# Kernel optimization log

Hardware: AMD Instinct MI355X
Metric: run time of the kernel (lower is better)

Reference implementation:

```python
import jax, jax.numpy as jnp
import numpy as np

N_SAMPLES = 2 ** 15  # 32768
NYQUIST = 22050.0 / 2.0
MIN_FREQ = 40.0 / NYQUIST
MAX_FREQ = 4000.0 / NYQUIST
FREQ_RANGE = MAX_FREQ - MIN_FREQ


def interp_linear(x, out_size):
    """torch F.interpolate(mode='linear', align_corners=False) along last axis."""
    in_size = x.shape[-1]
    scale = in_size / out_size
    coords = (jnp.arange(out_size, dtype=x.dtype) + 0.5) * scale - 0.5
    coords = jnp.clip(coords, 0.0, in_size - 1)
    lo = jnp.floor(coords).astype(jnp.int32)
    hi = jnp.minimum(lo + 1, in_size - 1)
    w = coords - lo.astype(x.dtype)
    return x[..., lo] * (1.0 - w) + x[..., hi] * w


def translate(pair, shift, scale):
    # angle of complex(pair[:,:,0], pair[:,:,1]) / pi, then affine
    angle = jnp.arctan2(pair[:, :, 1, :], pair[:, :, 0, :]) / np.pi
    return shift + angle * scale


def setup_inputs() -> dict:
    key = jax.random.key(0)
    k1, k2 = jax.random.split(key)
    x = jax.random.normal(k1, (16, 8, 10, 128), dtype=jnp.float32)
    noise = jax.random.normal(k2, (16, 8, N_SAMPLES), dtype=jnp.float32)
    return {"x": x, "noise": noise}


def reference(x, noise):
    # x: (batch, n_osc, 10, time_ctrl); noise: (batch, n_osc, N_SAMPLES)
    basic = x[:, :, 0:2, :]
    amp = jnp.sqrt(jnp.sum(basic * basic, axis=2))            # (b, o, t)
    amp = interp_linear(amp, N_SAMPLES)                       # (b, o, N)

    f0 = translate(basic, MIN_FREQ, FREQ_RANGE)               # control-rate
    mix = interp_linear(translate(x[:, :, 2:4, :], 1.0, 0.5), N_SAMPLES)
    harm_amp = amp * mix
    noise_amp = amp * (1.0 - mix)

    noise_std = translate(x[:, :, 4:6, :], MIN_FREQ, FREQ_RANGE)
    mod_factor = translate(x[:, :, 6:8, :], 0.25, 4.75)
    b = translate(x[:, :, 8:10, :], 0.1, 9.9)

    # band_filtered_noise: narrowband noise as a frequency-jittered sine
    f0_fr = interp_linear(f0, N_SAMPLES)
    std_fr = interp_linear(noise_std, N_SAMPLES)
    bfn = jnp.sin(jnp.cumsum(f0_fr + noise * std_fr, axis=-1))
    noise_sig = noise_amp * bfn

    mod_factor = interp_linear(mod_factor, N_SAMPLES)
    b = interp_linear(b, N_SAMPLES)
    mod = b * jnp.sin(jnp.cumsum(mod_factor, axis=-1))
    sig = harm_amp * jnp.sin(jnp.cumsum(f0_fr, axis=-1) + mod)

    mixed = noise_sig + sig                                   # (b, o, N)
    return jnp.mean(mixed, axis=1, keepdims=True)             # (b, 1, N)
```

## Files before the change

### kernel.cpp

```cpp
#include <hip/hip_runtime.h>
#include <math.h>

#define NS    32768
#define NB    128
#define NSEQ  128
#define TPB1  256
#define NPART 32
#define PART  (NS / NPART)
#define TPB2  256
#define CH    4

__device__ __forceinline__ float fsin(double x) {
    double u = x * 0.15915494309189533576888376337251;
    double f = u - rint(u);
    return __builtin_amdgcn_sinf((float)f);
}

__device__ __forceinline__ void seg_params(int ci0, int& lo, int& hi,
                                           double& w0, double& wst) {
    if (ci0 < 128)            { lo = 0;   hi = 1;   w0 = 0.0; wst = 0.0; }
    else if (ci0 >= NS - 128) { lo = 127; hi = 127; w0 = 0.0; wst = 0.0; }
    else {
        lo = (ci0 - 128) >> 8;  hi = lo + 1;
        int off = (ci0 - 128) & 255;
        w0 = (off + 0.5) * (1.0 / 256.0);
        wst = 1.0 / 256.0;
    }
}

__global__ __launch_bounds__(TPB1)
void pre_kernel(const float* __restrict__ xg, const float* __restrict__ ng,
                double* __restrict__ wacc, double* __restrict__ wbins) {
    __shared__ double bins[6][NB];
    __shared__ double lred[TPB1 / 64][3];

    const double PI_  = 3.14159265358979323846;
    const double MINF = 40.0 / 11025.0;
    const double FRNG = (4000.0 - 40.0) / 11025.0;

    int s    = blockIdx.x;
    int tid  = threadIdx.x;
    int lane = tid & 63;
    int wid  = tid >> 6;

    const float* xs = xg + s * 10 * 128;
    double* gb = wbins + (size_t)s * 6 * NB;
    for (int idx = tid; idx < 6 * NB; idx += TPB1) {
        int q = idx >> 7, j = idx & 127;
        double v;
        if (q == 0) {
            double a0 = (double)xs[j], a1 = (double)xs[128 + j];
            v = sqrt(a0 * a0 + a1 * a1);
        } else {
            int c = (q - 1) * 2;
            double yy = (double)xs[(c + 1) * 128 + j];
            double xx = (double)xs[c * 128 + j];
            double ang = atan2(yy, xx) / PI_;
            double sh, sc;
            if      (q == 1) { sh = MINF; sc = FRNG; }
            else if (q == 2) { sh = 1.0;  sc = 0.5;  }
            else if (q == 3) { sh = MINF; sc = FRNG; }
            else if (q == 4) { sh = 0.25; sc = 4.75; }
            else             { sh = 0.1;  sc = 9.9;  }
            v = sh + ang * sc;
        }
        bins[q][j] = v;
        gb[q * NB + j] = v;
    }
    __syncthreads();

    int c   = tid;
    int ci0 = c * 128;
    int lo, hi; double w0, wst;
    seg_params(ci0, lo, hi, w0, wst);
    double f0L = bins[1][lo], dF0 = bins[1][hi] - f0L;
    double stL = bins[3][lo], dSt = bins[3][hi] - stL;
    double mfL = bins[4][lo], dMf = bins[4][hi] - mfL;

    const float4* nn4 = reinterpret_cast<const float4*>(ng + (size_t)s * NS + ci0);
    double S0 = 0.0, S1 = 0.0;
    #pragma unroll
    for (int q4 = 0; q4 < 32; ++q4) {
        float4 nv = nn4[q4];
        double jd = (double)(q4 * 4);
        S0 += (double)nv.x; S1 += jd * (double)nv.x;
        S0 += (double)nv.y; S1 += (jd + 1.0) * (double)nv.y;
        S0 += (double)nv.z; S1 += (jd + 2.0) * (double)nv.z;
        S0 += (double)nv.w; S1 += (jd + 3.0) * (double)nv.w;
    }
    double sw = 128.0 * w0 + wst * 8128.0;
    double t3 = 128.0 * f0L + dF0 * sw;
    double t2 = 128.0 * mfL + dMf * sw;
    double t1 = t3 + stL * S0 + dSt * (w0 * S0 + wst * S1);

    double v1 = t1, v3 = t3, v2 = t2;
    #pragma unroll
    for (int d = 1; d < 64; d <<= 1) {
        double u1 = __shfl_up(v1, d);
        double u3 = __shfl_up(v3, d);
        double u2 = __shfl_up(v2, d);
        if (lane >= d) { v1 += u1; v3 += u3; v2 += u2; }
    }
    if (lane == 63) { lred[wid][0] = v1; lred[wid][1] = v3; lred[wid][2] = v2; }
    __syncthreads();
    double b1 = 0.0, b3 = 0.0, b2 = 0.0;
    #pragma unroll
    for (int k = 0; k < TPB1 / 64 - 1; ++k)
        if (wid > k) { b1 += lred[k][0]; b3 += lred[k][1]; b2 += lred[k][2]; }

    if ((c & 7) == 0) {
        double* A = wacc + ((size_t)s * NPART + (c >> 3)) * 3;
        A[0] = b1 + (v1 - t1);
        A[1] = b3 + (v3 - t3);
        A[2] = b2 + (v2 - t2);
    }
}

__global__ __launch_bounds__(TPB2)
void fm_main_kernel(const float* __restrict__ ng, const double* __restrict__ wacc,
                    const double* __restrict__ wbins, float* __restrict__ out) {
    __shared__ double lbins[8][6][NB];
    __shared__ double lred[TPB2 / 64][3];

    int bx   = blockIdx.x;
    int b    = bx >> 5;
    int p    = bx & (NPART - 1);
    int tid  = threadIdx.x;
    int lane = tid & 63;
    int wid  = tid >> 6;

    const double* gb = wbins + (size_t)b * 8 * 6 * NB;
    double* lb = &lbins[0][0][0];
    for (int idx = tid; idx < 8 * 6 * NB; idx += TPB2) lb[idx] = gb[idx];
    __syncthreads();

    int i0 = p * PART + tid * CH;
    int lo, hi; double w0, wst;
    seg_params(i0, lo, hi, w0, wst);

    float acc[CH] = {0.f, 0.f, 0.f, 0.f};

    for (int h = 0; h < 8; ++h) {
        int s = b * 8 + h;
        const double* B = &lbins[h][0][0];
        double amL = B[0 * NB + lo], dAm = B[0 * NB + hi] - amL;
        double f0L = B[1 * NB + lo], dF0 = B[1 * NB + hi] - f0L;
        double mxL = B[2 * NB + lo], dMx = B[2 * NB + hi] - mxL;
        double stL = B[3 * NB + lo], dSt = B[3 * NB + hi] - stL;
        double mfL = B[4 * NB + lo], dMf = B[4 * NB + hi] - mfL;
        double bL  = B[5 * NB + lo], dB  = B[5 * NB + hi] - bL;

        float4 nv = *reinterpret_cast<const float4*>(ng + (size_t)s * NS + i0);
        double n0 = (double)nv.x, n1 = (double)nv.y, n2 = (double)nv.z, n3 = (double)nv.w;
        double S0 = n0 + n1 + n2 + n3;
        double S1 = n1 + 2.0 * n2 + 3.0 * n3;

        double sw = 4.0 * w0 + wst * 6.0;
        double T3 = 4.0 * f0L + dF0 * sw;
        double T2 = 4.0 * mfL + dMf * sw;
        double T1 = T3 + stL * S0 + dSt * (w0 * S0 + wst * S1);

        double v1 = T1, v3 = T3, v2 = T2;
        #pragma unroll
        for (int d = 1; d < 64; d <<= 1) {
            double u1 = __shfl_up(v1, d);
            double u3 = __shfl_up(v3, d);
            double u2 = __shfl_up(v2, d);
            if (lane >= d) { v1 += u1; v3 += u3; v2 += u2; }
        }
        if (lane == 63) { lred[wid][0] = v1; lred[wid][1] = v3; lred[wid][2] = v2; }
        __syncthreads();
        double b1 = 0.0, b3 = 0.0, b2 = 0.0;
        #pragma unroll
        for (int k = 0; k < TPB2 / 64 - 1; ++k)
            if (wid > k) { b1 += lred[k][0]; b3 += lred[k][1]; b2 += lred[k][2]; }
        __syncthreads();

        const double* A = wacc + ((size_t)s * NPART + p) * 3;
        double a1 = A[0] + b1 + (v1 - T1);
        double a3 = A[1] + b3 + (v3 - T3);
        double a2 = A[2] + b2 + (v2 - T2);

        float nf[CH] = {nv.x, nv.y, nv.z, nv.w};
        double w = w0;
        #pragma unroll
        for (int j = 0; j < CH; ++j) {
            double nd  = (double)nf[j];
            double f0v = f0L + w * dF0;
            double stv = stL + w * dSt;
            double mfv = mfL + w * dMf;
            a1 += f0v + nd * stv;
            a3 += f0v;
            a2 += mfv;
            double ampv = amL + w * dAm;
            double mixv = mxL + w * dMx;
            double bv   = bL  + w * dB;
            double harm = ampv * mixv;
            double namp = ampv * (1.0 - mixv);
            float s1 = fsin(a1);
            float s2 = fsin(a2);
            float s3 = fsin(a3 + bv * (double)s2);
            acc[j] += (float)namp * s1 + (float)harm * s3;
            w += wst;
        }
    }

    float4 o = make_float4(acc[0] * 0.125f, acc[1] * 0.125f,
                           acc[2] * 0.125f, acc[3] * 0.125f);
    *reinterpret_cast<float4*>(out + (size_t)b * NS + i0) = o;
}

extern "C" void kernel_launch(void* const* d_in, const int* in_sizes, int n_in,
                              void* d_out, int out_size, void* d_ws, size_t ws_size,
                              hipStream_t stream) {
    const float* x     = (const float*)d_in[0];
    const float* noise = (const float*)d_in[1];
    float* out = (float*)d_out;
    double* wacc  = (double*)d_ws;
    double* wbins = wacc + (size_t)NSEQ * NPART * 3;
    pre_kernel<<<NSEQ, TPB1, 0, stream>>>(x, noise, wacc, wbins);
    fm_main_kernel<<<16 * NPART, TPB2, 0, stream>>>(noise, wacc, wbins, out);
}
```

Baseline: 95.86 us.

## Precompute per-16-sample phase offsets and run main synthesis in fp32

The pre-kernel now computes exclusive prefix phase sums at 16-sample granularity using 1024 threads, with phases pre-scaled by 1/(2π) and reduced modulo 1. This removes the per-oscillator block-wide double scans and barriers from the main kernel. The main kernel instead assigns one thread per (cell, oscillator), does the local accumulation and interpolation in fp32, and sums the 8 oscillators with xor shuffles. It trades double-precision work and syncs for more workspace traffic and fp32 rounding inside each cell.

```diff
diff --git a/kernel.cpp b/kernel.cpp
--- a/kernel.cpp
+++ b/kernel.cpp
@@ -4,25 +4,24 @@
 #define NS    32768
 #define NB    128
 #define NSEQ  128
-#define TPB1  256
-#define NPART 32
-#define PART  (NS / NPART)
+#define CELL  16
+#define NCELL (NS / CELL)
+#define TPB1  1024
+#define RUN   (NS / TPB1)
 #define TPB2  256
-#define CH    4
-
-__device__ __forceinline__ float fsin(double x) {
-    double u = x * 0.15915494309189533576888376337251;
-    double f = u - rint(u);
-    return __builtin_amdgcn_sinf((float)f);
-}
-
-__device__ __forceinline__ void seg_params(int ci0, int& lo, int& hi,
+#define GRID2 (16 * NCELL * 8 / TPB2)
+
+__device__ __forceinline__ float sinr(float x) {
+    return __builtin_amdgcn_sinf(x - rintf(x));
+}
+
+__device__ __forceinline__ void seg_params(int i, int& lo, int& hi,
                                            double& w0, double& wst) {
-    if (ci0 < 128)            { lo = 0;   hi = 1;   w0 = 0.0; wst = 0.0; }
-    else if (ci0 >= NS - 128) { lo = 127; hi = 127; w0 = 0.0; wst = 0.0; }
+    if (i < 128)            { lo = 0;   hi = 1;   w0 = 0.0; wst = 0.0; }
+    else if (i >= NS - 128) { lo = 127; hi = 127; w0 = 0.0; wst = 0.0; }
     else {
-        lo = (ci0 - 128) >> 8;  hi = lo + 1;
-        int off = (ci0 - 128) & 255;
+        lo = (i - 128) >> 8;  hi = lo + 1;
+        int off = (i - 128) & 255;
         w0 = (off + 0.5) * (1.0 / 256.0);
         wst = 1.0 / 256.0;
     }
@@ -30,32 +29,31 @@
 
 __global__ __launch_bounds__(TPB1)
 void pre_kernel(const float* __restrict__ xg, const float* __restrict__ ng,
-                double* __restrict__ wacc, double* __restrict__ wbins) {
-    __shared__ double bins[6][NB];
+                double* __restrict__ wacc, float* __restrict__ wbins) {
+    __shared__ double bf0[NB], bst[NB], bmf[NB];
     __shared__ double lred[TPB1 / 64][3];
 
-    const double PI_  = 3.14159265358979323846;
-    const double MINF = 40.0 / 11025.0;
-    const double FRNG = (4000.0 - 40.0) / 11025.0;
+    const double PI_    = 3.14159265358979323846;
+    const double INV2PI = 0.15915494309189533576888376337251;
+    const double MINF   = 40.0 / 11025.0;
+    const double FRNG   = (4000.0 - 40.0) / 11025.0;
 
     int s    = blockIdx.x;
     int tid  = threadIdx.x;
     int lane = tid & 63;
     int wid  = tid >> 6;
 
-    const float* xs = xg + s * 10 * 128;
-    double* gb = wbins + (size_t)s * 6 * NB;
-    for (int idx = tid; idx < 6 * NB; idx += TPB1) {
-        int q = idx >> 7, j = idx & 127;
+    const float* xs = xg + s * 10 * NB;
+    if (tid < 6 * NB) {
+        int q = tid >> 7, j = tid & 127;
         double v;
         if (q == 0) {
-            double a0 = (double)xs[j], a1 = (double)xs[128 + j];
+            double a0 = (double)xs[j], a1 = (double)xs[NB + j];
             v = sqrt(a0 * a0 + a1 * a1);
         } else {
-            int c = (q - 1) * 2;
-            double yy = (double)xs[(c + 1) * 128 + j];
-            double xx = (double)xs[c * 128 + j];
-            double ang = atan2(yy, xx) / PI_;
+            int c2 = (q - 1) * 2;
+            double ang = atan2((double)xs[(c2 + 1) * NB + j],
+                               (double)xs[c2 * NB + j]) / PI_;
             double sh, sc;
             if      (q == 1) { sh = MINF; sc = FRNG; }
             else if (q == 2) { sh = 1.0;  sc = 0.5;  }
@@ -63,37 +61,46 @@
             else if (q == 4) { sh = 0.25; sc = 4.75; }
             else             { sh = 0.1;  sc = 9.9;  }
             v = sh + ang * sc;
+            if (q != 2) v *= INV2PI;
         }
-        bins[q][j] = v;
-        gb[q * NB + j] = v;
+        wbins[s * (6 * NB) + tid] = (float)v;
+        if      (q == 1) bf0[j] = v;
+        else if (q == 3) bst[j] = v;
+        else if (q == 4) bmf[j] = v;
     }
     __syncthreads();
 
-    int c   = tid;
-    int ci0 = c * 128;
+    int ci = tid * RUN;
     int lo, hi; double w0, wst;
-    seg_params(ci0, lo, hi, w0, wst);
-    double f0L = bins[1][lo], dF0 = bins[1][hi] - f0L;
-    double stL = bins[3][lo], dSt = bins[3][hi] - stL;
-    double mfL = bins[4][lo], dMf = bins[4][hi] - mfL;
-
-    const float4* nn4 = reinterpret_cast<const float4*>(ng + (size_t)s * NS + ci0);
-    double S0 = 0.0, S1 = 0.0;
-    #pragma unroll
-    for (int q4 = 0; q4 < 32; ++q4) {
-        float4 nv = nn4[q4];
-        double jd = (double)(q4 * 4);
-        S0 += (double)nv.x; S1 += jd * (double)nv.x;
-        S0 += (double)nv.y; S1 += (jd + 1.0) * (double)nv.y;
-        S0 += (double)nv.z; S1 += (jd + 2.0) * (double)nv.z;
-        S0 += (double)nv.w; S1 += (jd + 3.0) * (double)nv.w;
-    }
-    double sw = 128.0 * w0 + wst * 8128.0;
-    double t3 = 128.0 * f0L + dF0 * sw;
-    double t2 = 128.0 * mfL + dMf * sw;
-    double t1 = t3 + stL * S0 + dSt * (w0 * S0 + wst * S1);
-
-    double v1 = t1, v3 = t3, v2 = t2;
+    seg_params(ci, lo, hi, w0, wst);
+    double f0L = bf0[lo], dF0 = bf0[hi] - f0L;
+    double stL = bst[lo], dSt = bst[hi] - stL;
+    double mfL = bmf[lo], dMf = bmf[hi] - mfL;
+
+    const float4* nn4 = reinterpret_cast<const float4*>(ng + (size_t)s * NS + ci);
+    double t1c[2], t3c[2], t2c[2];
+    #pragma unroll
+    for (int c = 0; c < 2; ++c) {
+        double S0 = 0.0, S1 = 0.0;
+        #pragma unroll
+        for (int q4 = 0; q4 < 4; ++q4) {
+            float4 nv = nn4[c * 4 + q4];
+            double jd = (double)(q4 * 4);
+            S0 += (double)nv.x; S1 += jd * (double)nv.x;
+            S0 += (double)nv.y; S1 += (jd + 1.0) * (double)nv.y;
+            S0 += (double)nv.z; S1 += (jd + 2.0) * (double)nv.z;
+            S0 += (double)nv.w; S1 += (jd + 3.0) * (double)nv.w;
+        }
+        double wc = w0 + (double)(c * 16) * wst;
+        double sw = 16.0 * wc + wst * 120.0;
+        double t3 = 16.0 * f0L + dF0 * sw;
+        double t2 = 16.0 * mfL + dMf * sw;
+        double t1 = t3 + stL * S0 + dSt * (wc * S0 + wst * S1);
+        t1c[c] = t1; t3c[c] = t3; t2c[c] = t2;
+    }
+    double r1 = t1c[0] + t1c[1], r3 = t3c[0] + t3c[1], r2 = t2c[0] + t2c[1];
+
+    double v1 = r1, v3 = r3, v2 = r2;
     #pragma unroll
     for (int d = 1; d < 64; d <<= 1) {
         double u1 = __shfl_up(v1, d);
@@ -104,110 +111,84 @@
     if (lane == 63) { lred[wid][0] = v1; lred[wid][1] = v3; lred[wid][2] = v2; }
     __syncthreads();
     double b1 = 0.0, b3 = 0.0, b2 = 0.0;
-    #pragma unroll
-    for (int k = 0; k < TPB1 / 64 - 1; ++k)
-        if (wid > k) { b1 += lred[k][0]; b3 += lred[k][1]; b2 += lred[k][2]; }
-
-    if ((c & 7) == 0) {
-        double* A = wacc + ((size_t)s * NPART + (c >> 3)) * 3;
-        A[0] = b1 + (v1 - t1);
-        A[1] = b3 + (v3 - t3);
-        A[2] = b2 + (v2 - t2);
-    }
+    for (int k = 0; k < wid; ++k) {
+        b1 += lred[k][0]; b3 += lred[k][1]; b2 += lred[k][2];
+    }
+    double e1 = b1 + v1 - r1, e3 = b3 + v3 - r3, e2 = b2 + v2 - r2;
+
+    double* A = wacc + ((size_t)s * NCELL + (size_t)tid * 2) * 3;
+    A[0] = e1;          A[1] = e3;          A[2] = e2;
+    A[3] = e1 + t1c[0]; A[4] = e3 + t3c[0]; A[5] = e2 + t2c[0];
 }
 
 __global__ __launch_bounds__(TPB2)
-void fm_main_kernel(const float* __restrict__ ng, const double* __restrict__ wacc,
-                    const double* __restrict__ wbins, float* __restrict__ out) {
-    __shared__ double lbins[8][6][NB];
-    __shared__ double lred[TPB2 / 64][3];
-
-    int bx   = blockIdx.x;
-    int b    = bx >> 5;
-    int p    = bx & (NPART - 1);
-    int tid  = threadIdx.x;
-    int lane = tid & 63;
-    int wid  = tid >> 6;
-
-    const double* gb = wbins + (size_t)b * 8 * 6 * NB;
-    double* lb = &lbins[0][0][0];
-    for (int idx = tid; idx < 8 * 6 * NB; idx += TPB2) lb[idx] = gb[idx];
-    __syncthreads();
-
-    int i0 = p * PART + tid * CH;
-    int lo, hi; double w0, wst;
-    seg_params(i0, lo, hi, w0, wst);
-
-    float acc[CH] = {0.f, 0.f, 0.f, 0.f};
-
-    for (int h = 0; h < 8; ++h) {
-        int s = b * 8 + h;
-        const double* B = &lbins[h][0][0];
-        double amL = B[0 * NB + lo], dAm = B[0 * NB + hi] - amL;
-        double f0L = B[1 * NB + lo], dF0 = B[1 * NB + hi] - f0L;
-        double mxL = B[2 * NB + lo], dMx = B[2 * NB + hi] - mxL;
-        double stL = B[3 * NB + lo], dSt = B[3 * NB + hi] - stL;
-        double mfL = B[4 * NB + lo], dMf = B[4 * NB + hi] - mfL;
-        double bL  = B[5 * NB + lo], dB  = B[5 * NB + hi] - bL;
-
-        float4 nv = *reinterpret_cast<const float4*>(ng + (size_t)s * NS + i0);
-        double n0 = (double)nv.x, n1 = (double)nv.y, n2 = (double)nv.z, n3 = (double)nv.w;
-        double S0 = n0 + n1 + n2 + n3;
-        double S1 = n1 + 2.0 * n2 + 3.0 * n3;
-
-        double sw = 4.0 * w0 + wst * 6.0;
-        double T3 = 4.0 * f0L + dF0 * sw;
-        double T2 = 4.0 * mfL + dMf * sw;
-        double T1 = T3 + stL * S0 + dSt * (w0 * S0 + wst * S1);
-
-        double v1 = T1, v3 = T3, v2 = T2;
+void fm2_kernel(const float* __restrict__ ng, const double* __restrict__ wacc,
+                const float* __restrict__ wbins, float* __restrict__ out) {
+    int g  = blockIdx.x * TPB2 + threadIdx.x;
+    int h  = g & 7;
+    int q  = g >> 3;
+    int b  = q >> 11;
+    int c  = q & (NCELL - 1);
+    int s  = (b << 3) + h;
+    int i0 = c << 4;
+
+    int lo, hi; double w0d, wstd;
+    seg_params(i0, lo, hi, w0d, wstd);
+    float w0  = (float)w0d;
+    float wsf = (float)wstd;
+
+    const float* B = wbins + s * (6 * NB);
+    float amL = B[lo],          dAm = B[hi] - amL;
+    float f0L = B[NB + lo],     dF0 = B[NB + hi] - f0L;
+    float mxL = B[2 * NB + lo], dMx = B[2 * NB + hi] - mxL;
+    float stL = B[3 * NB + lo], dSt = B[3 * NB + hi] - stL;
+    float mfL = B[4 * NB + lo], dMf = B[4 * NB + hi] - mfL;
+    float bbL = B[5 * NB + lo], dBb = B[5 * NB + hi] - bbL;
+
+    const double* A = wacc + ((size_t)s * NCELL + c) * 3;
+    double a1 = A[0], a3 = A[1], a2 = A[2];
+    float fr1 = (float)(a1 - rint(a1));
+    float fr3 = (float)(a3 - rint(a3));
+    float fr2 = (float)(a2 - rint(a2));
+
+    const float4* nn4 = reinterpret_cast<const float4*>(ng + (size_t)s * NS + i0);
+    float4 nv0 = nn4[0], nv1 = nn4[1], nv2 = nn4[2], nv3 = nn4[3];
+    float nf[CELL] = {nv0.x, nv0.y, nv0.z, nv0.w, nv1.x, nv1.y, nv1.z, nv1.w,
+                      nv2.x, nv2.y, nv2.z, nv2.w, nv3.x, nv3.y, nv3.z, nv3.w};
+
+    float arr[CELL];
+    float d1 = 0.f, d2 = 0.f, d3 = 0.f;
+    #pragma unroll
+    for (int j = 0; j < CELL; ++j) {
+        float wf  = fmaf((float)j, wsf, w0);
+        float f0v = fmaf(wf, dF0, f0L);
+        float stv = fmaf(wf, dSt, stL);
+        float mfv = fmaf(wf, dMf, mfL);
+        d3 += f0v;
+        d1 += fmaf(nf[j], stv, f0v);
+        d2 += mfv;
+        float ampv = fmaf(wf, dAm, amL);
+        float mixv = fmaf(wf, dMx, mxL);
+        float bv   = fmaf(wf, dBb, bbL);
+        float s2 = sinr(fr2 + d2);
+        float s1 = sinr(fr1 + d1);
+        float s3 = sinr(fmaf(bv, s2, fr3 + d3));
+        float harm = ampv * mixv;
+        arr[j] = fmaf(harm, s3, (ampv - harm) * s1);
+    }
+
+    #pragma unroll
+    for (int m = 1; m <= 4; m <<= 1) {
         #pragma unroll
-        for (int d = 1; d < 64; d <<= 1) {
-            double u1 = __shfl_up(v1, d);
-            double u3 = __shfl_up(v3, d);
-            double u2 = __shfl_up(v2, d);
-            if (lane >= d) { v1 += u1; v3 += u3; v2 += u2; }
-        }
-        if (lane == 63) { lred[wid][0] = v1; lred[wid][1] = v3; lred[wid][2] = v2; }
-        __syncthreads();
-        double b1 = 0.0, b3 = 0.0, b2 = 0.0;
+        for (int j = 0; j < CELL; ++j) arr[j] += __shfl_xor(arr[j], m);
+    }
+    if (h == 0) {
+        float4* op = reinterpret_cast<float4*>(out + (size_t)b * NS + i0);
         #pragma unroll
-        for (int k = 0; k < TPB2 / 64 - 1; ++k)
-            if (wid > k) { b1 += lred[k][0]; b3 += lred[k][1]; b2 += lred[k][2]; }
-        __syncthreads();
-
-        const double* A = wacc + ((size_t)s * NPART + p) * 3;
-        double a1 = A[0] + b1 + (v1 - T1);
-        double a3 = A[1] + b3 + (v3 - T3);
-        double a2 = A[2] + b2 + (v2 - T2);
-
-        float nf[CH] = {nv.x, nv.y, nv.z, nv.w};
-        double w = w0;
-        #pragma unroll
-        for (int j = 0; j < CH; ++j) {
-            double nd  = (double)nf[j];
-            double f0v = f0L + w * dF0;
-            double stv = stL + w * dSt;
-            double mfv = mfL + w * dMf;
-            a1 += f0v + nd * stv;
-            a3 += f0v;
-            a2 += mfv;
-            double ampv = amL + w * dAm;
-            double mixv = mxL + w * dMx;
-            double bv   = bL  + w * dB;
-            double harm = ampv * mixv;
-            double namp = ampv * (1.0 - mixv);
-            float s1 = fsin(a1);
-            float s2 = fsin(a2);
-            float s3 = fsin(a3 + bv * (double)s2);
-            acc[j] += (float)namp * s1 + (float)harm * s3;
-            w += wst;
-        }
-    }
-
-    float4 o = make_float4(acc[0] * 0.125f, acc[1] * 0.125f,
-                           acc[2] * 0.125f, acc[3] * 0.125f);
-    *reinterpret_cast<float4*>(out + (size_t)b * NS + i0) = o;
+        for (int j4 = 0; j4 < 4; ++j4)
+            op[j4] = make_float4(arr[j4 * 4 + 0] * 0.125f, arr[j4 * 4 + 1] * 0.125f,
+                                 arr[j4 * 4 + 2] * 0.125f, arr[j4 * 4 + 3] * 0.125f);
+    }
 }
 
 extern "C" void kernel_launch(void* const* d_in, const int* in_sizes, int n_in,
@@ -216,8 +197,8 @@
     const float* x     = (const float*)d_in[0];
     const float* noise = (const float*)d_in[1];
     float* out = (float*)d_out;
-    double* wacc  = (double*)d_ws;
-    double* wbins = wacc + (size_t)NSEQ * NPART * 3;
+    double* wacc = (double*)d_ws;
+    float* wbins = (float*)(wacc + (size_t)NSEQ * NCELL * 3);
     pre_kernel<<<NSEQ, TPB1, 0, stream>>>(x, noise, wacc, wbins);
-    fm_main_kernel<<<16 * NPART, TPB2, 0, stream>>>(noise, wacc, wbins, out);
-}
+    fm2_kernel<<<GRID2, TPB2, 0, stream>>>(noise, wacc, wbins, out);
+}
```

Measured after the change: 81.37 us. 1.18x faster.
